# Kernel optimization log

Measured on AMD Instinct MI355X. Metric: run time of the kernel, lower is better.

Reference implementation:

```python
import jax, jax.numpy as jnp
import numpy as np

B, L1, L, DIM_IN, DIM_H, DIM_M = 8, 64, 1024, 512, 512, 512


def setup_inputs() -> dict:
    key = jax.random.key(0)
    ks = jax.random.split(key, 7)
    return {
        "query": jax.random.normal(ks[0], (L1, DIM_H), dtype=jnp.float32),
        "keys": jax.random.normal(ks[1], (B, L, DIM_IN), dtype=jnp.float32),
        "values": jax.random.normal(ks[2], (B, L, DIM_IN), dtype=jnp.float32),
        # nn.Linear weights: Wx (dim_middle, dim_in) no bias; Wh (dim_middle, dim_h) with bias; w (dim_middle,) no bias
        "Wx": jax.random.normal(ks[3], (DIM_M, DIM_IN), dtype=jnp.float32) * 0.02,
        "Wh": jax.random.normal(ks[4], (DIM_M, DIM_H), dtype=jnp.float32) * 0.02,
        "bh": jax.random.normal(ks[5], (DIM_M,), dtype=jnp.float32) * 0.02,
        "w": jax.random.normal(ks[6], (DIM_M,), dtype=jnp.float32) * 0.02,
    }


def reference(query, keys, values, Wx, Wh, bh, w):
    # mode='concept': query [l1, dh], keys/values [b, l, d]
    kx = jnp.einsum('bld,md->blm', keys, Wx)          # [b, l, m]
    qh = jnp.einsum('qd,md->qm', query, Wh) + bh       # [l1, m]
    g = jax.nn.relu(kx[:, None, :, :] + qh[None, :, None, :])  # [b, l1, l, m]
    scores = jnp.einsum('bqlm,m->bql', g, w)           # [b, l1, l]
    e = jax.nn.softmax(scores, axis=-1)                # softmax over key len (dim 2)
    return jnp.einsum('bql,bld->bqd', e, values)       # [b, l1, dv]
```

## Files before the change

### kernel.cpp

```cpp
#include <hip/hip_runtime.h>
#include <hip/hip_bf16.h>

#define BB 8
#define L1 64
#define LL 1024
#define DD 512

typedef float f32x4 __attribute__((ext_vector_type(4)));
typedef _Float16 f16;
typedef _Float16 f16x2 __attribute__((ext_vector_type(2)));
typedef _Float16 f16x4 __attribute__((ext_vector_type(4)));
typedef _Float16 f16x8 __attribute__((ext_vector_type(8)));

union F16x8u { f16x8 v; f16x2 h[4]; };
union U4H8 { uint4 u; f16x8 v; };

__global__ __launch_bounds__(256) void kxqh_kernel(
    const float* __restrict__ keys,
    const float* __restrict__ query,
    const float* __restrict__ Wx,
    const float* __restrict__ Wh,
    const float* __restrict__ bh,
    f16* __restrict__ kx,
    f16* __restrict__ qh) {
  __shared__ char lds[49152] __attribute__((aligned(128)));
  const int t = threadIdx.x;
  const int lane = t & 63;
  const int w = t >> 6;
  const int fq = lane >> 4, fr = lane & 15;
  const int bid = blockIdx.x;

  if (bid < 8) {
    const int m0 = bid * 64;
    const int wid = w;
    f32x4 acc[4] = {};
    float4 rq[4], rw[4];
#define LOADQ(KC)                                                              \
    do {                                                                       \
      _Pragma("unroll") for (int i = 0; i < 4; ++i) {                          \
        int slot = t + i * 256;                                                \
        int row = slot >> 4, c4 = (slot & 15) * 4;                             \
        rq[i] = *reinterpret_cast<const float4*>(query + (size_t)row * DD + (KC)*64 + c4); \
        rw[i] = *reinterpret_cast<const float4*>(Wh + (size_t)(m0 + row) * DD + (KC)*64 + c4); \
      }                                                                        \
    } while (0)
    LOADQ(0);
    for (int kc = 0; kc < 8; ++kc) {
      #pragma unroll
      for (int i = 0; i < 4; ++i) {
        int slot = t + i * 256;
        int row = slot >> 4, c4 = (slot & 15) * 4;
        f16x4 hq, hw;
        hq[0] = (f16)rq[i].x; hq[1] = (f16)rq[i].y; hq[2] = (f16)rq[i].z; hq[3] = (f16)rq[i].w;
        hw[0] = (f16)rw[i].x; hw[1] = (f16)rw[i].y; hw[2] = (f16)rw[i].z; hw[3] = (f16)rw[i].w;
        *reinterpret_cast<f16x4*>(lds + row * 144 + c4 * 2) = hq;
        *reinterpret_cast<f16x4*>(lds + 9216 + row * 144 + c4 * 2) = hw;
      }
      if (kc < 7) LOADQ(kc + 1);
      __syncthreads();
      #pragma unroll
      for (int kh = 0; kh < 2; ++kh) {
        f16x8 bf = *reinterpret_cast<const f16x8*>(
            lds + 9216 + (wid * 16 + fr) * 144 + kh * 64 + fq * 16);
        #pragma unroll
        for (int qf = 0; qf < 4; ++qf) {
          f16x8 af = *reinterpret_cast<const f16x8*>(
              lds + (qf * 16 + fr) * 144 + kh * 64 + fq * 16);
          acc[qf] = __builtin_amdgcn_mfma_f32_16x16x32_f16(af, bf, acc[qf], 0, 0, 0);
        }
      }
      __syncthreads();
    }
#undef LOADQ
    #pragma unroll
    for (int qf = 0; qf < 4; ++qf) {
      int m = m0 + wid * 16 + fr;
      float bias = bh[m];
      #pragma unroll
      for (int r = 0; r < 4; ++r)
        qh[(size_t)(qf * 16 + fq * 4 + r) * DD + m] = (f16)(acc[qf][r] + bias);
    }
    return;
  }

  const int kb = bid - 8;
  const int rt = kb & 127;
  const int mt = kb >> 7;
  const int rowA0 = rt * 64;
  const int m0 = mt * 128;
  const int wr = w >> 1, wc = w & 1;

  f32x4 acc[2][4] = {};
  float4 ra[4], rb[8];

#define LOADK(K0)                                                              \
  do {                                                                         \
    _Pragma("unroll") for (int i = 0; i < 4; ++i) {                            \
      int flat = t * 4 + i * 1024;                                             \
      int row = flat >> 6, col = flat & 63;                                    \
      ra[i] = *reinterpret_cast<const float4*>(keys + (size_t)(rowA0 + row) * DD + (K0) + col); \
    }                                                                          \
    _Pragma("unroll") for (int i = 0; i < 8; ++i) {                            \
      int flat = t * 4 + i * 1024;                                             \
      int row = flat >> 6, col = flat & 63;                                    \
      rb[i] = *reinterpret_cast<const float4*>(Wx + (size_t)(m0 + row) * DD + (K0) + col); \
    }                                                                          \
  } while (0)

  LOADK(0);
  for (int s = 0; s < 8; ++s) {
    const int base = (s & 1) * 24576;
    #pragma unroll
    for (int i = 0; i < 4; ++i) {
      int flat = t * 4 + i * 1024;
      int row = flat >> 6, col = flat & 63;
      f16x4 ha;
      ha[0] = (f16)ra[i].x; ha[1] = (f16)ra[i].y; ha[2] = (f16)ra[i].z; ha[3] = (f16)ra[i].w;
      *reinterpret_cast<f16x4*>(lds + base + row * 128 + ((col * 2) ^ ((row & 7) << 4))) = ha;
    }
    #pragma unroll
    for (int i = 0; i < 8; ++i) {
      int flat = t * 4 + i * 1024;
      int row = flat >> 6, col = flat & 63;
      f16x4 hb;
      hb[0] = (f16)rb[i].x; hb[1] = (f16)rb[i].y; hb[2] = (f16)rb[i].z; hb[3] = (f16)rb[i].w;
      *reinterpret_cast<f16x4*>(lds + base + 8192 + row * 128 + ((col * 2) ^ ((row & 7) << 4))) = hb;
    }
    if (s < 7) LOADK((s + 1) * 64);
    __syncthreads();
    #pragma unroll
    for (int kh = 0; kh < 2; ++kh) {
      f16x8 af[2], bf[4];
      #pragma unroll
      for (int mi = 0; mi < 2; ++mi) {
        int row = wr * 32 + mi * 16 + fr;
        af[mi] = *reinterpret_cast<const f16x8*>(
            lds + base + row * 128 + ((kh * 64 + fq * 16) ^ ((row & 7) << 4)));
      }
      #pragma unroll
      for (int ni = 0; ni < 4; ++ni) {
        int row = wc * 64 + ni * 16 + fr;
        bf[ni] = *reinterpret_cast<const f16x8*>(
            lds + base + 8192 + row * 128 + ((kh * 64 + fq * 16) ^ ((row & 7) << 4)));
      }
      #pragma unroll
      for (int mi = 0; mi < 2; ++mi)
        #pragma unroll
        for (int ni = 0; ni < 4; ++ni)
          acc[mi][ni] = __builtin_amdgcn_mfma_f32_16x16x32_f16(
              af[mi], bf[ni], acc[mi][ni], 0, 0, 0);
    }
  }
#undef LOADK
  #pragma unroll
  for (int mi = 0; mi < 2; ++mi) {
    #pragma unroll
    for (int ni = 0; ni < 4; ++ni) {
      int row = rowA0 + wr * 32 + mi * 16 + fq * 4;
      int col = m0 + wc * 64 + ni * 16 + fr;
      #pragma unroll
      for (int r = 0; r < 4; ++r)
        kx[(size_t)(row + r) * DD + col] = (f16)acc[mi][ni][r];
    }
  }
}

__global__ __launch_bounds__(512) void score6_kernel(
    const f16* __restrict__ kx,
    const f16* __restrict__ qh,
    const float* __restrict__ w,
    f16* __restrict__ sc,
    float* __restrict__ pmax) {
  const int b = blockIdx.x & 7;
  const int l0 = (blockIdx.x >> 3) * 32;
  const int t = threadIdx.x;
  __shared__ __align__(16) char kxs[32 * 256];
  __shared__ __align__(16) char qhs[64 * 256];
  __shared__ __align__(16) f16 wsf[DD];
  __shared__ float smax[64][17];
  if (t < 128) {
    float4 wv = *reinterpret_cast<const float4*>(w + t * 4);
    f16x4 hv; hv[0] = (f16)wv.x; hv[1] = (f16)wv.y; hv[2] = (f16)wv.z; hv[3] = (f16)wv.w;
    *reinterpret_cast<f16x4*>(&wsf[t * 4]) = hv;
  }
  const int qb = t & 31;
  const int lp = t >> 5;
  float acc[2][2] = {};
  uint4 rkx, rqh[2];

#define LOADM(M0)                                                              \
  do {                                                                         \
    {                                                                          \
      int row = t >> 4, col = (t & 15) * 8;                                    \
      rkx = *reinterpret_cast<const uint4*>(kx + (size_t)(b * LL + l0 + row) * DD + (M0) + col); \
    }                                                                          \
    _Pragma("unroll") for (int p = 0; p < 2; ++p) {                            \
      int slot = t + p * 512;                                                  \
      int row = slot >> 4, col = (slot & 15) * 8;                              \
      rqh[p] = *reinterpret_cast<const uint4*>(qh + (size_t)row * DD + (M0) + col); \
    }                                                                          \
  } while (0)

  LOADM(0);
  for (int m0 = 0; m0 < DD; m0 += 128) {
    {
      int row = t >> 4, cb = (t & 15) * 16;
      *reinterpret_cast<uint4*>(kxs + row * 256 + (cb ^ ((row & 7) << 4))) = rkx;
    }
    #pragma unroll
    for (int p = 0; p < 2; ++p) {
      int slot = t + p * 512;
      int row = slot >> 4, cb = (slot & 15) * 16;
      *reinterpret_cast<uint4*>(qhs + row * 256 + (cb ^ ((row & 7) << 4))) = rqh[p];
    }
    if (m0 < DD - 128) LOADM(m0 + 128);
    __syncthreads();
    #pragma unroll 2
    for (int mm = 0; mm < 128; mm += 8) {
      const int mb = mm * 2;
      F16x8u kv0, kv1, wv;
      {
        int r0 = lp * 2, r1 = lp * 2 + 1;
        kv0.v = *reinterpret_cast<const f16x8*>(kxs + r0 * 256 + (mb ^ ((r0 & 7) << 4)));
        kv1.v = *reinterpret_cast<const f16x8*>(kxs + r1 * 256 + (mb ^ ((r1 & 7) << 4)));
      }
      wv.v = *reinterpret_cast<const f16x8*>(&wsf[m0 + mm]);
      #pragma unroll
      for (int j = 0; j < 2; ++j) {
        int qr = qb + 32 * j;
        F16x8u qv, g0, g1;
        qv.v = *reinterpret_cast<const f16x8*>(qhs + qr * 256 + (mb ^ ((qr & 7) << 4)));
        f16x8 zz = {};
        g0.v = __builtin_elementwise_max(kv0.v + qv.v, zz);
        g1.v = __builtin_elementwise_max(kv1.v + qv.v, zz);
        #pragma unroll
        for (int c = 0; c < 4; ++c) {
          acc[0][j] = __builtin_amdgcn_fdot2(g0.h[c], wv.h[c], acc[0][j], false);
          acc[1][j] = __builtin_amdgcn_fdot2(g1.h[c], wv.h[c], acc[1][j], false);
        }
      }
    }
    __syncthreads();
  }
#undef LOADM
  #pragma unroll
  for (int i = 0; i < 2; ++i)
    #pragma unroll
    for (int j = 0; j < 2; ++j)
      sc[((size_t)b * L1 + qb + 32 * j) * LL + l0 + lp * 2 + i] = (f16)acc[i][j];
  #pragma unroll
  for (int j = 0; j < 2; ++j)
    smax[qb + 32 * j][lp] = fmaxf(acc[0][j], acc[1][j]);
  __syncthreads();
  if (t < 64) {
    float m = smax[t][0];
    #pragma unroll
    for (int i = 1; i < 16; ++i) m = fmaxf(m, smax[t][i]);
    pmax[((size_t)b * L1 + t) * 32 + (l0 >> 5)] = m;
  }
}

__global__ __launch_bounds__(512) void fso3_kernel(
    const f16* __restrict__ sc,
    const float* __restrict__ pmax,
    const float* __restrict__ v,
    float* __restrict__ out) {
  __shared__ __align__(16) char es[64 * 256];
  __shared__ __align__(16) char vt[16 * 256];
  __shared__ float rowm[64];
  __shared__ float rowinv[64];
  __shared__ float spart[64][17];
  __shared__ f32x4 accbuf[4][64];
  const int t = threadIdx.x;
  const int lane = t & 63;
  const int w = t >> 6;
  const int fq = lane >> 4, fr = lane & 15;
  const int bid = blockIdx.x;
  const int b = bid & 7;
  const int d0 = (bid >> 3) * 16;
  const f16* scb = sc + (size_t)b * L1 * LL;
  const float* vb = v + (size_t)b * LL * DD;

  const int r0 = t >> 4;
  const int r1 = (t + 512) >> 4;
  const int ec8 = t & 15;
  const int vl = t >> 2;
  const int dq = (t & 3) * 4;
  uint4 rsc[2];
  float4 rv;

#define LOADC(LC)                                                              \
  do {                                                                         \
    rsc[0] = *reinterpret_cast<const uint4*>(scb + (size_t)r0 * LL + (LC) * 128 + ec8 * 8); \
    rsc[1] = *reinterpret_cast<const uint4*>(scb + (size_t)r1 * LL + (LC) * 128 + ec8 * 8); \
    rv = *reinterpret_cast<const float4*>(                                     \
        vb + (size_t)((LC) * 128 + vl) * DD + d0 + dq);                        \
  } while (0)

  LOADC(0);
  if (t < 64) {
    const float* pm = pmax + ((size_t)b * L1 + t) * 32;
    float4 m4 = *reinterpret_cast<const float4*>(pm);
    #pragma unroll
    for (int i = 1; i < 8; ++i) {
      float4 x = *reinterpret_cast<const float4*>(pm + i * 4);
      m4.x = fmaxf(m4.x, x.x); m4.y = fmaxf(m4.y, x.y);
      m4.z = fmaxf(m4.z, x.z); m4.w = fmaxf(m4.w, x.w);
    }
    rowm[t] = fmaxf(fmaxf(m4.x, m4.y), fmaxf(m4.z, m4.w));
  }
  __syncthreads();
  float rmv[2] = {rowm[r0], rowm[r1]};
  float spp[2] = {0.f, 0.f};
  f32x4 acc = {};
  const int qs = (w & 3) * 16;
  const int ksh = (w >> 2) * 2;

  for (int c = 0; c < 8; ++c) {
    #pragma unroll
    for (int p = 0; p < 2; ++p) {
      int q = p ? r1 : r0;
      U4H8 x; x.u = rsc[p];
      f16x8 h;
      #pragma unroll
      for (int j = 0; j < 8; ++j) {
        float e = __expf((float)x.v[j] - rmv[p]);
        spp[p] += e;
        h[j] = (f16)e;
      }
      int byte = q * 256 + ((ec8 * 16) ^ ((q & 7) << 4));
      *reinterpret_cast<f16x8*>(es + byte) = h;
    }
    {
      float vs[4] = {rv.x, rv.y, rv.z, rv.w};
      #pragma unroll
      for (int j = 0; j < 4; ++j) {
        int d = dq + j;
        int byte = d * 256 + ((2 * vl) ^ ((d & 7) << 4));
        *reinterpret_cast<f16*>(vt + byte) = (f16)vs[j];
      }
    }
    if (c < 7) LOADC(c + 1);
    __syncthreads();
    #pragma unroll
    for (int ki = 0; ki < 2; ++ki) {
      int ks = ksh + ki;
      int qa = qs + fr;
      int colb = ks * 64 + fq * 16;
      f16x8 a = *reinterpret_cast<const f16x8*>(es + qa * 256 + (colb ^ ((qa & 7) << 4)));
      f16x8 bb = *reinterpret_cast<const f16x8*>(vt + fr * 256 + (colb ^ ((fr & 7) << 4)));
      acc = __builtin_amdgcn_mfma_f32_16x16x32_f16(a, bb, acc, 0, 0, 0);
    }
    __syncthreads();
  }
#undef LOADC
  spart[r0][ec8] = spp[0];
  spart[r1][ec8] = spp[1];
  if (w >= 4) accbuf[w & 3][lane] = acc;
  __syncthreads();
  if (t < 64) {
    float S = 0.f;
    #pragma unroll
    for (int i = 0; i < 16; ++i) S += spart[t][i];
    rowinv[t] = 1.f / S;
  }
  __syncthreads();
  if (w < 4) {
    f32x4 ah = accbuf[w][lane];
    acc += ah;
    #pragma unroll
    for (int r = 0; r < 4; ++r) {
      int q = qs + fq * 4 + r;
      out[((size_t)b * L1 + q) * DD + d0 + fr] = acc[r] * rowinv[q];
    }
  }
}

extern "C" void kernel_launch(void* const* d_in, const int* in_sizes, int n_in,
                              void* d_out, int out_size, void* d_ws, size_t ws_size,
                              hipStream_t stream) {
  const float* query  = (const float*)d_in[0];
  const float* keys   = (const float*)d_in[1];
  const float* values = (const float*)d_in[2];
  const float* Wx     = (const float*)d_in[3];
  const float* Wh     = (const float*)d_in[4];
  const float* bh     = (const float*)d_in[5];
  const float* w      = (const float*)d_in[6];
  float* out = (float*)d_out;

  char* ws = (char*)d_ws;
  f16*   kx   = (f16*)ws;
  f16*   qh   = (f16*)(ws + 8388608);
  f16*   sc   = (f16*)(ws + 8454144);
  float* pmax = (float*)(ws + 9502720);

  kxqh_kernel<<<520, 256, 0, stream>>>(keys, query, Wx, Wh, bh, kx, qh);
  score6_kernel<<<256, 512, 0, stream>>>(kx, qh, w, sc, pmax);
  fso3_kernel<<<256, 512, 0, stream>>>(sc, pmax, values, out);
}
```

Baseline: 48.81 us.

## Move softmax into a dedicated row-normalization kernel before the PV matmul

```diff
diff --git a/kernel.cpp b/kernel.cpp
--- a/kernel.cpp
+++ b/kernel.cpp
@@ -165,19 +165,17 @@
   }
 }
 
-__global__ __launch_bounds__(512) void score6_kernel(
+__global__ __launch_bounds__(512) void score7_kernel(
     const f16* __restrict__ kx,
     const f16* __restrict__ qh,
     const float* __restrict__ w,
-    f16* __restrict__ sc,
-    float* __restrict__ pmax) {
+    f16* __restrict__ sc) {
   const int b = blockIdx.x & 7;
   const int l0 = (blockIdx.x >> 3) * 32;
   const int t = threadIdx.x;
   __shared__ __align__(16) char kxs[32 * 256];
   __shared__ __align__(16) char qhs[64 * 256];
   __shared__ __align__(16) f16 wsf[DD];
-  __shared__ float smax[64][17];
   if (t < 128) {
     float4 wv = *reinterpret_cast<const float4*>(w + t * 4);
     f16x4 hv; hv[0] = (f16)wv.x; hv[1] = (f16)wv.y; hv[2] = (f16)wv.z; hv[3] = (f16)wv.w;
@@ -248,28 +246,48 @@
     #pragma unroll
     for (int j = 0; j < 2; ++j)
       sc[((size_t)b * L1 + qb + 32 * j) * LL + l0 + lp * 2 + i] = (f16)acc[i][j];
-  #pragma unroll
-  for (int j = 0; j < 2; ++j)
-    smax[qb + 32 * j][lp] = fmaxf(acc[0][j], acc[1][j]);
-  __syncthreads();
-  if (t < 64) {
-    float m = smax[t][0];
-    #pragma unroll
-    for (int i = 1; i < 16; ++i) m = fmaxf(m, smax[t][i]);
-    pmax[((size_t)b * L1 + t) * 32 + (l0 >> 5)] = m;
-  }
-}
-
-__global__ __launch_bounds__(512) void fso3_kernel(
+}
+
+__global__ __launch_bounds__(64) void esn_kernel(
     const f16* __restrict__ sc,
-    const float* __restrict__ pmax,
+    f16* __restrict__ esn) {
+  const int row = blockIdx.x;
+  const int lane = threadIdx.x;
+  const f16* s = sc + (size_t)row * LL + lane * 16;
+  U4H8 a, bv;
+  a.u = reinterpret_cast<const uint4*>(s)[0];
+  bv.u = reinterpret_cast<const uint4*>(s)[1];
+  float x[16];
+  #pragma unroll
+  for (int j = 0; j < 8; ++j) { x[j] = (float)a.v[j]; x[8 + j] = (float)bv.v[j]; }
+  float m = x[0];
+  #pragma unroll
+  for (int j = 1; j < 16; ++j) m = fmaxf(m, x[j]);
+  #pragma unroll
+  for (int off = 32; off > 0; off >>= 1) m = fmaxf(m, __shfl_xor(m, off));
+  float ssum = 0.f;
+  #pragma unroll
+  for (int j = 0; j < 16; ++j) { x[j] = __expf(x[j] - m); ssum += x[j]; }
+  #pragma unroll
+  for (int off = 32; off > 0; off >>= 1) ssum += __shfl_xor(ssum, off);
+  const float inv = 1.f / ssum;
+  U4H8 o0, o1;
+  #pragma unroll
+  for (int j = 0; j < 8; ++j) {
+    o0.v[j] = (f16)(x[j] * inv);
+    o1.v[j] = (f16)(x[8 + j] * inv);
+  }
+  uint4* d = reinterpret_cast<uint4*>(esn + (size_t)row * LL + lane * 16);
+  d[0] = o0.u;
+  d[1] = o1.u;
+}
+
+__global__ __launch_bounds__(512) void pv_kernel(
+    const f16* __restrict__ esn,
     const float* __restrict__ v,
     float* __restrict__ out) {
   __shared__ __align__(16) char es[64 * 256];
   __shared__ __align__(16) char vt[16 * 256];
-  __shared__ float rowm[64];
-  __shared__ float rowinv[64];
-  __shared__ float spart[64][17];
   __shared__ f32x4 accbuf[4][64];
   const int t = threadIdx.x;
   const int lane = t & 63;
@@ -278,7 +296,7 @@
   const int bid = blockIdx.x;
   const int b = bid & 7;
   const int d0 = (bid >> 3) * 16;
-  const f16* scb = sc + (size_t)b * L1 * LL;
+  const f16* scb = esn + (size_t)b * L1 * LL;
   const float* vb = v + (size_t)b * LL * DD;
 
   const int r0 = t >> 4;
@@ -298,38 +316,16 @@
   } while (0)
 
   LOADC(0);
-  if (t < 64) {
-    const float* pm = pmax + ((size_t)b * L1 + t) * 32;
-    float4 m4 = *reinterpret_cast<const float4*>(pm);
-    #pragma unroll
-    for (int i = 1; i < 8; ++i) {
-      float4 x = *reinterpret_cast<const float4*>(pm + i * 4);
-      m4.x = fmaxf(m4.x, x.x); m4.y = fmaxf(m4.y, x.y);
-      m4.z = fmaxf(m4.z, x.z); m4.w = fmaxf(m4.w, x.w);
-    }
-    rowm[t] = fmaxf(fmaxf(m4.x, m4.y), fmaxf(m4.z, m4.w));
-  }
-  __syncthreads();
-  float rmv[2] = {rowm[r0], rowm[r1]};
-  float spp[2] = {0.f, 0.f};
   f32x4 acc = {};
   const int qs = (w & 3) * 16;
   const int ksh = (w >> 2) * 2;
 
   for (int c = 0; c < 8; ++c) {
-    #pragma unroll
-    for (int p = 0; p < 2; ++p) {
-      int q = p ? r1 : r0;
-      U4H8 x; x.u = rsc[p];
-      f16x8 h;
-      #pragma unroll
-      for (int j = 0; j < 8; ++j) {
-        float e = __expf((float)x.v[j] - rmv[p]);
-        spp[p] += e;
-        h[j] = (f16)e;
-      }
-      int byte = q * 256 + ((ec8 * 16) ^ ((q & 7) << 4));
-      *reinterpret_cast<f16x8*>(es + byte) = h;
+    {
+      int byte0 = r0 * 256 + ((ec8 * 16) ^ ((r0 & 7) << 4));
+      *reinterpret_cast<uint4*>(es + byte0) = rsc[0];
+      int byte1 = r1 * 256 + ((ec8 * 16) ^ ((r1 & 7) << 4));
+      *reinterpret_cast<uint4*>(es + byte1) = rsc[1];
     }
     {
       float vs[4] = {rv.x, rv.y, rv.z, rv.w};
@@ -354,16 +350,7 @@
     __syncthreads();
   }
 #undef LOADC
-  spart[r0][ec8] = spp[0];
-  spart[r1][ec8] = spp[1];
   if (w >= 4) accbuf[w & 3][lane] = acc;
-  __syncthreads();
-  if (t < 64) {
-    float S = 0.f;
-    #pragma unroll
-    for (int i = 0; i < 16; ++i) S += spart[t][i];
-    rowinv[t] = 1.f / S;
-  }
   __syncthreads();
   if (w < 4) {
     f32x4 ah = accbuf[w][lane];
@@ -371,7 +358,7 @@
     #pragma unroll
     for (int r = 0; r < 4; ++r) {
       int q = qs + fq * 4 + r;
-      out[((size_t)b * L1 + q) * DD + d0 + fr] = acc[r] * rowinv[q];
+      out[((size_t)b * L1 + q) * DD + d0 + fr] = acc[r];
     }
   }
 }
@@ -389,12 +376,13 @@
   float* out = (float*)d_out;
 
   char* ws = (char*)d_ws;
-  f16*   kx   = (f16*)ws;
-  f16*   qh   = (f16*)(ws + 8388608);
-  f16*   sc   = (f16*)(ws + 8454144);
-  float* pmax = (float*)(ws + 9502720);
+  f16* kx  = (f16*)ws;
+  f16* qh  = (f16*)(ws + 8388608);
+  f16* sc  = (f16*)(ws + 8454144);
+  f16* esn = (f16*)(ws + 9502720);
 
   kxqh_kernel<<<520, 256, 0, stream>>>(keys, query, Wx, Wh, bh, kx, qh);
-  score6_kernel<<<256, 512, 0, stream>>>(kx, qh, w, sc, pmax);
-  fso3_kernel<<<256, 512, 0, stream>>>(sc, pmax, values, out);
-}
+  score7_kernel<<<256, 512, 0, stream>>>(kx, qh, w, sc);
+  esn_kernel<<<BB * L1, 64, 0, stream>>>(sc, esn);
+  pv_kernel<<<256, 512, 0, stream>>>(esn, values, out);
+}
```

Result: slower. 74.89 us (+53.4%).
